# Performance work log

Measured on AMD Instinct MI355X. Metric: run time of the kernel, lower is better.

The kernel has to match this reference:

```python
import jax, jax.numpy as jnp
import numpy as np

B, L, D = 2048, 100, 128          # batch, early_cycle_threshold, d_model
F = L * D                          # flattened curve features = 12800
DLLM, DFF, E, K = 768, 256, 8, 2   # d_llm, d_ff, num_experts, top_k
EPS = 1e-9


def setup_inputs() -> dict:
    key = jax.random.key(0)
    ks = jax.random.split(key, 12)
    gin = DLLM + 1 + F  # gate input dim: concat(DKP, cycle_number, flat curve)
    return {
        "cycle_curve_data": jax.random.normal(ks[0], (B, L, D), jnp.float32),
        "cycle_numbers": jax.random.uniform(ks[1], (B, 1), jnp.float32) * 100.0,
        "DKP_embeddings": jax.random.normal(ks[2], (B, DLLM), jnp.float32),
        # gate MLP (PatternRouter_three): concat -> d_ff -> gelu -> num_experts
        "Wg1": jax.random.normal(ks[3], (gin, DFF), jnp.float32) / np.sqrt(gin),
        "bg1": jnp.zeros((DFF,), jnp.float32),
        "Wg2": jax.random.normal(ks[4], (DFF, E), jnp.float32) / np.sqrt(DFF),
        "bg2": jnp.zeros((E,), jnp.float32),
        # per-expert Linear(F, d_model)
        "We": jax.random.normal(ks[5], (E, F, D), jnp.float32) / np.sqrt(F),
        "be": jnp.zeros((E, D), jnp.float32),
        # general expert Linear(F, d_model)
        "Wgen": jax.random.normal(ks[6], (F, D), jnp.float32) / np.sqrt(F),
        "bgen": jnp.zeros((D,), jnp.float32),
    }


def reference(cycle_curve_data, cycle_numbers, DKP_embeddings,
              Wg1, bg1, Wg2, bg2, We, be, Wgen, bgen):
    b = cycle_curve_data.shape[0]
    xf = cycle_curve_data.reshape(b, -1)  # [B, F]

    # gate logits: MLP on concat(DKP, cycle_numbers, flattened curve)
    gin = jnp.concatenate([DKP_embeddings, cycle_numbers, xf], axis=-1)
    h = jax.nn.gelu(gin @ Wg1 + bg1)
    logits = h @ Wg2 + bg2                # [B, E]

    # top-k mask, softmax over ALL experts, then mask + renormalize
    _, idx = jax.lax.top_k(logits, K)     # [B, K]
    mask = jnp.sum(jax.nn.one_hot(idx, E, dtype=logits.dtype), axis=1)  # [B, E]
    probs = jax.nn.softmax(logits, axis=-1)
    masked = probs * mask
    gates = masked / (jnp.sum(masked, axis=-1, keepdims=True) + EPS)  # [B, E]

    # experts: dense compute, zero gates nullify unselected experts (same math
    # as gather-compute-scatter dispatch/combine)
    expert_outs = jnp.einsum('bf,efd->bed', xf, We) + be   # [B, E, D]
    combined = jnp.einsum('be,bed->bd', gates, expert_outs)
    combined = combined.astype(jnp.bfloat16)               # torch .to(bfloat16)

    general = xf @ Wgen + bgen                              # [B, D] f32
    final_out = general + combined.astype(general.dtype)    # bf16+f32 -> f32
    return final_out
```

## Files before the change

kernel.cpp:

```cpp
#include <hip/hip_runtime.h>
#include <hip/hip_bf16.h>
#include <stdint.h>

#define B_    2048
#define F_    12800
#define DLLM_ 768
#define E_    8
#define G1Z   32
#define MKSPLIT 8
#define MKPER (F_ / MKSPLIT)
#define BK    64

typedef __bf16 bf16x8 __attribute__((ext_vector_type(8)));
typedef float  f32x4  __attribute__((ext_vector_type(4)));

__device__ __forceinline__ unsigned short f2bf(float f) {
    unsigned int u = __float_as_uint(f);
    u += 0x7fffu + ((u >> 16) & 1u);
    return (unsigned short)(u >> 16);
}

__global__ __launch_bounds__(256) void k_convert(const float* __restrict__ src,
                                                 unsigned short* __restrict__ dst, int n4) {
    int i = blockIdx.x * 256 + threadIdx.x;
    if (i >= n4) return;
    float4 v = ((const float4*)src)[i];
    ushort4 o;
    o.x = f2bf(v.x); o.y = f2bf(v.y); o.z = f2bf(v.z); o.w = f2bf(v.w);
    ((ushort4*)dst)[i] = o;
}

__global__ __launch_bounds__(256) void k_transpose_bf16(const float* __restrict__ We,
                                                        const float* __restrict__ Wgen,
                                                        unsigned short* __restrict__ WeT,
                                                        unsigned short* __restrict__ WgenT) {
    __shared__ float t[32][33];
    int z = blockIdx.z;
    const float* src = (z < 8) ? (We + (size_t)z * F_ * 128) : Wgen;
    unsigned short* dst = (z < 8) ? (WeT + (size_t)z * 128 * F_) : WgenT;
    int k0 = blockIdx.x * 32, n0 = blockIdx.y * 32;
    int tx = threadIdx.x, ty = threadIdx.y;
#pragma unroll
    for (int i = 0; i < 4; i++) {
        int k = k0 + ty + i * 8;
        t[ty + i * 8][tx] = src[(size_t)k * 128 + n0 + tx];
    }
    __syncthreads();
#pragma unroll
    for (int i = 0; i < 4; i++) {
        int n = n0 + ty + i * 8;
        dst[(size_t)n * F_ + k0 + tx] = f2bf(t[tx][ty + i * 8]);
    }
}

__global__ __launch_bounds__(256, 2) void k_gate1(const float* __restrict__ dkp,
                                                  const float* __restrict__ xf,
                                                  const float* __restrict__ Wg1,
                                                  float* __restrict__ h_part,
                                                  int nparts) {
    __shared__ float As[16][132];
    __shared__ float Bs[16][260];
    int m0 = blockIdx.x * 128;
    int s = blockIdx.y;
    int it0 = s * 26 + (s < 16 ? s : 16);
    int nit = 26 + (s < 16 ? 1 : 0);
    int t = threadIdx.x;
    int tm = t >> 5;
    int tn = t & 31;

    float acc[16][8];
#pragma unroll
    for (int i = 0; i < 16; i++)
#pragma unroll
        for (int j = 0; j < 8; j++) acc[i][j] = 0.f;

    int arow = t >> 2, akq = (t & 3) * 4;
    int bkr = t >> 6, bcol = (t & 63) * 4;

    float4 aR[2], bR[4];
    auto preload = [&](int k) {
        const float* Ab; int astr, aoff, wr0;
        if (k < DLLM_) { Ab = dkp; astr = DLLM_; aoff = k; wr0 = k; }
        else           { Ab = xf;  astr = F_;    aoff = k - DLLM_; wr0 = k + 1; }
        aR[0] = *(const float4*)&Ab[(size_t)(m0 + arow) * astr + aoff + akq];
        aR[1] = *(const float4*)&Ab[(size_t)(m0 + arow + 64) * astr + aoff + akq];
#pragma unroll
        for (int r = 0; r < 4; r++)
            bR[r] = *(const float4*)&Wg1[(size_t)(wr0 + bkr + r * 4) * 256 + bcol];
    };
    preload(it0 * 16);
    for (int it = 0; it < nit; it++) {
        __syncthreads();
        {
            float a0[4] = {aR[0].x, aR[0].y, aR[0].z, aR[0].w};
            float a1[4] = {aR[1].x, aR[1].y, aR[1].z, aR[1].w};
#pragma unroll
            for (int j = 0; j < 4; j++) {
                As[akq + j][arow]      = a0[j];
                As[akq + j][arow + 64] = a1[j];
            }
#pragma unroll
            for (int r = 0; r < 4; r++)
                *(float4*)&Bs[bkr + r * 4][bcol] = bR[r];
        }
        __syncthreads();
        if (it + 1 < nit) preload((it0 + it + 1) * 16);
#pragma unroll 4
        for (int kk = 0; kk < 16; kk++) {
            float4 a0 = *(const float4*)&As[kk][tm * 16];
            float4 a1 = *(const float4*)&As[kk][tm * 16 + 4];
            float4 a2 = *(const float4*)&As[kk][tm * 16 + 8];
            float4 a3 = *(const float4*)&As[kk][tm * 16 + 12];
            float4 b0 = *(const float4*)&Bs[kk][tn * 8];
            float4 b1 = *(const float4*)&Bs[kk][tn * 8 + 4];
            float av[16] = {a0.x, a0.y, a0.z, a0.w, a1.x, a1.y, a1.z, a1.w,
                            a2.x, a2.y, a2.z, a2.w, a3.x, a3.y, a3.z, a3.w};
            float bv[8]  = {b0.x, b0.y, b0.z, b0.w, b1.x, b1.y, b1.z, b1.w};
#pragma unroll
            for (int i = 0; i < 16; i++)
#pragma unroll
                for (int j = 0; j < 8; j++) acc[i][j] = fmaf(av[i], bv[j], acc[i][j]);
        }
    }
    if (nparts > 1) {
        float* dst = h_part + (size_t)s * B_ * 256;
#pragma unroll
        for (int i = 0; i < 16; i++) {
            size_t base = (size_t)(m0 + tm * 16 + i) * 256 + tn * 8;
            *(float4*)&dst[base]     = (float4){acc[i][0], acc[i][1], acc[i][2], acc[i][3]};
            *(float4*)&dst[base + 4] = (float4){acc[i][4], acc[i][5], acc[i][6], acc[i][7]};
        }
    } else {
#pragma unroll
        for (int i = 0; i < 16; i++) {
            size_t base = (size_t)(m0 + tm * 16 + i) * 256 + tn * 8;
#pragma unroll
            for (int j = 0; j < 8; j++) atomicAdd(&h_part[base + j], acc[i][j]);
        }
    }
}

__global__ __launch_bounds__(256) void k_gate2(const float* __restrict__ h_part,
                                               const float* __restrict__ cyc,
                                               const float* __restrict__ Wg1,
                                               const float* __restrict__ bg1,
                                               const float* __restrict__ Wg2,
                                               const float* __restrict__ bg2,
                                               float* __restrict__ gates,
                                               unsigned int* __restrict__ cnt,
                                               unsigned int* __restrict__ rows,
                                               int nparts) {
    __shared__ float hs[8 * 257];
    __shared__ float w2s[256 * 8];
    __shared__ float ls[8][9];
    int r0 = blockIdx.x * 8;
    int t = threadIdx.x;
    const float* w768 = Wg1 + (size_t)DLLM_ * 256;
    float wc = w768[t], b1c = bg1[t];
#pragma unroll
    for (int i = 0; i < 8; i++) {
        size_t idx = (size_t)(r0 + i) * 256 + t;
        float x = 0.f;
        for (int p = 0; p < nparts; p++) x += h_part[(size_t)p * B_ * 256 + idx];
        x += cyc[r0 + i] * wc + b1c;
        float x3 = x * x * x;
        float g = 0.5f * x * (1.f + tanhf(0.7978845608028654f * (x + 0.044715f * x3)));
        hs[i * 257 + t] = g;
    }
#pragma unroll
    for (int i = 0; i < 8; i++) w2s[i * 256 + t] = Wg2[i * 256 + t];
    __syncthreads();
    if (t < 64) {
        int r = t >> 3, e = t & 7;
        float s = bg2[e];
        for (int k2 = 0; k2 < 256; k2++) s = fmaf(hs[r * 257 + k2], w2s[k2 * 8 + e], s);
        ls[r][e] = s;
    }
    __syncthreads();
    if (t < 8) {
        float l[8];
#pragma unroll
        for (int e = 0; e < 8; e++) l[e] = ls[t][e];
        int i1 = 0; float v1 = l[0];
#pragma unroll
        for (int e = 1; e < 8; e++) if (l[e] > v1) { v1 = l[e]; i1 = e; }
        int i2 = -1; float v2 = -3.0e38f;
#pragma unroll
        for (int e = 0; e < 8; e++) if (e != i1 && l[e] > v2) { v2 = l[e]; i2 = e; }
        float p[8], ps = 0.f;
#pragma unroll
        for (int e = 0; e < 8; e++) { p[e] = expf(l[e] - v1); ps += p[e]; }
        float msum = (p[i1] + p[i2]) / ps;
        float gi = 1.f / (msum + 1e-9f);
        int row = r0 + t;
#pragma unroll
        for (int e = 0; e < 8; e++) {
            float ge = (e == i1 || e == i2) ? (p[e] / ps) * gi : 0.f;
            gates[row * 8 + e] = ge;
        }
        unsigned int s1 = atomicAdd(&cnt[i1], 1u); rows[i1 * 2048 + s1] = (unsigned int)row;
        unsigned int s2 = atomicAdd(&cnt[i2], 1u); rows[i2 * 2048 + s2] = (unsigned int)row;
    }
}

__global__ __launch_bounds__(256) void k_moe(const unsigned short* __restrict__ xfb,
                                             const unsigned short* __restrict__ WeT,
                                             const unsigned short* __restrict__ WgenT,
                                             const float* __restrict__ be,
                                             const float* __restrict__ gates,
                                             const unsigned int* __restrict__ cnt,
                                             const unsigned int* __restrict__ rows,
                                             float* __restrict__ comb,
                                             float* __restrict__ gen) {
    __shared__ unsigned short As[64 * 72];
    __shared__ unsigned short Bs[128 * 72];
    __shared__ unsigned int rowid_s[64];
    int e = blockIdx.y, tile = blockIdx.x, split = blockIdx.z;
    int n_rows = (e < 8) ? (int)cnt[e] : 2048;
    if (tile * 64 >= n_rows) return;
    int t = threadIdx.x;
    if (t < 64) {
        int m = tile * 64 + t;
        unsigned int row = (e < 8) ? ((m < n_rows) ? rows[e * 2048 + m] : rows[e * 2048])
                                   : (unsigned int)m;
        rowid_s[t] = row;
    }
    __syncthreads();
    const unsigned short* WT = (e < 8) ? (WeT + (size_t)e * 128 * F_) : WgenT;
    int k0 = split * MKPER;

    int arow = t >> 2, akq = t & 3;
    const unsigned short* aptr = xfb + (size_t)rowid_s[arow] * F_ + k0 + akq * 8;
    unsigned short* asd0 = &As[arow * 72 + akq * 8];
    unsigned short* asd1 = &As[arow * 72 + (akq + 4) * 8];
    int bcol = t >> 1, bh = t & 1;
    const unsigned short* bptr = WT + (size_t)bcol * F_ + k0 + bh * 32;
    unsigned short* bsd = &Bs[bcol * 72 + bh * 32];

    int lane = t & 63;
    int lm = lane & 15, lg = lane >> 4;
    int wave = t >> 6, wr = wave >> 1, wc2 = wave & 1;

    f32x4 acc[2][4];
#pragma unroll
    for (int i = 0; i < 2; i++)
#pragma unroll
        for (int j = 0; j < 4; j++) acc[i][j] = (f32x4){0.f, 0.f, 0.f, 0.f};

    uint4 ra0 = *(const uint4*)aptr;
    uint4 ra1 = *(const uint4*)(aptr + 32);
    uint4 rb0 = *(const uint4*)(bptr);
    uint4 rb1 = *(const uint4*)(bptr + 8);
    uint4 rb2 = *(const uint4*)(bptr + 16);
    uint4 rb3 = *(const uint4*)(bptr + 24);
    for (int kk = 0; kk < MKPER; kk += BK) {
        __syncthreads();
        *(uint4*)asd0 = ra0;
        *(uint4*)asd1 = ra1;
        *(uint4*)(bsd)      = rb0;
        *(uint4*)(bsd + 8)  = rb1;
        *(uint4*)(bsd + 16) = rb2;
        *(uint4*)(bsd + 24) = rb3;
        __syncthreads();
        if (kk + BK < MKPER) {
            aptr += BK; bptr += BK;
            ra0 = *(const uint4*)aptr;
            ra1 = *(const uint4*)(aptr + 32);
            rb0 = *(const uint4*)(bptr);
            rb1 = *(const uint4*)(bptr + 8);
            rb2 = *(const uint4*)(bptr + 16);
            rb3 = *(const uint4*)(bptr + 24);
        }
#pragma unroll
        for (int kb = 0; kb < 2; kb++) {
            bf16x8 af[2], bfr[4];
#pragma unroll
            for (int mt = 0; mt < 2; mt++)
                af[mt] = *(const bf16x8*)&As[(wr * 32 + mt * 16 + lm) * 72 + (kb * 4 + lg) * 8];
#pragma unroll
            for (int nt = 0; nt < 4; nt++)
                bfr[nt] = *(const bf16x8*)&Bs[(wc2 * 64 + nt * 16 + lm) * 72 + (kb * 4 + lg) * 8];
#pragma unroll
            for (int mt = 0; mt < 2; mt++)
#pragma unroll
                for (int nt = 0; nt < 4; nt++)
                    acc[mt][nt] = __builtin_amdgcn_mfma_f32_16x16x32_bf16(af[mt], bfr[nt], acc[mt][nt], 0, 0, 0);
        }
    }
#pragma unroll
    for (int mt = 0; mt < 2; mt++) {
        int rl0 = wr * 32 + mt * 16 + lg * 4;
#pragma unroll
        for (int nt = 0; nt < 4; nt++) {
            int col = wc2 * 64 + nt * 16 + lm;
#pragma unroll
            for (int r = 0; r < 4; r++) {
                int rloc = rl0 + r;
                float v = acc[mt][nt][r];
                if (e < 8) {
                    if (tile * 64 + rloc < n_rows) {
                        unsigned int grow = rowid_s[rloc];
                        float g = gates[grow * 8 + e];
                        float bias = (split == 0) ? be[e * 128 + col] : 0.f;
                        atomicAdd(&comb[(size_t)grow * 128 + col], g * (v + bias));
                    }
                } else {
                    atomicAdd(&gen[(size_t)(tile * 64 + rloc) * 128 + col], v);
                }
            }
        }
    }
}

__global__ __launch_bounds__(256) void k_final(const float* __restrict__ gen,
                                               const float* __restrict__ comb,
                                               const float* __restrict__ bgen,
                                               float* __restrict__ out) {
    int i = blockIdx.x * 256 + threadIdx.x;
    float g = gen[i] + bgen[i & 127];
    unsigned short cb = f2bf(comb[i]);
    float c = __uint_as_float(((unsigned int)cb) << 16);
    out[i] = g + c;
}

extern "C" void kernel_launch(void* const* d_in, const int* in_sizes, int n_in,
                              void* d_out, int out_size, void* d_ws, size_t ws_size,
                              hipStream_t stream) {
    (void)in_sizes; (void)n_in; (void)out_size;
    const float* ccd  = (const float*)d_in[0];
    const float* cyc  = (const float*)d_in[1];
    const float* dkp  = (const float*)d_in[2];
    const float* Wg1  = (const float*)d_in[3];
    const float* bg1  = (const float*)d_in[4];
    const float* Wg2  = (const float*)d_in[5];
    const float* bg2  = (const float*)d_in[6];
    const float* We   = (const float*)d_in[7];
    const float* be   = (const float*)d_in[8];
    const float* Wgen = (const float*)d_in[9];
    const float* bgen = (const float*)d_in[10];
    float* out = (float*)d_out;

    char* ws = (char*)d_ws;
    size_t o = 0;
    unsigned short* xfb   = (unsigned short*)(ws + o); o += (size_t)B_ * F_ * 2;
    unsigned short* WeT   = (unsigned short*)(ws + o); o += (size_t)E_ * 128 * F_ * 2;
    unsigned short* WgenT = (unsigned short*)(ws + o); o += (size_t)128 * F_ * 2;
    float* gates = (float*)(ws + o); o += (size_t)B_ * 8 * 4;
    unsigned int* cnt = (unsigned int*)(ws + o); o += 256;
    unsigned int* rows = (unsigned int*)(ws + o); o += (size_t)8 * 2048 * 4;
    float* comb = (float*)(ws + o); o += (size_t)B_ * 128 * 4;
    float* gen  = (float*)(ws + o); o += (size_t)B_ * 128 * 4;
    float* h_part = (float*)(ws + o);
    size_t need_full = o + (size_t)G1Z * B_ * 256 * 4;
    int nparts = (ws_size >= need_full) ? G1Z : 1;

    if (nparts == 1)
        hipMemsetAsync(h_part, 0, (size_t)B_ * 256 * 4, stream);
    hipMemsetAsync(comb, 0, (size_t)B_ * 128 * 4, stream);
    hipMemsetAsync(gen,  0, (size_t)B_ * 128 * 4, stream);
    hipMemsetAsync(cnt,  0, 32, stream);

    k_convert<<<(B_ * F_ / 4) / 256, 256, 0, stream>>>(ccd, xfb, B_ * F_ / 4);
    k_transpose_bf16<<<dim3(F_ / 32, 4, 9), dim3(32, 8, 1), 0, stream>>>(We, Wgen, WeT, WgenT);
    k_gate1<<<dim3(16, G1Z), 256, 0, stream>>>(dkp, ccd, Wg1, h_part, nparts);
    k_gate2<<<B_ / 8, 256, 0, stream>>>(h_part, cyc, Wg1, bg1, Wg2, bg2, gates, cnt, rows, nparts);
    k_moe<<<dim3(32, 9, MKSPLIT), 256, 0, stream>>>(xfb, WeT, WgenT, be, gates, cnt, rows, comb, gen);
    k_final<<<(B_ * 128) / 256, 256, 0, stream>>>(gen, comb, bgen, out);
}
```

Measured before the change: 652.1 us.

## Replace MoE atomics with per-split partial buffers and remap gate1 B-tile columns

The MoE kernel now writes split-K and top-k-slot partial results into separate buffers, reusing the gate partial region, instead of doing atomicAdd into comb/gen. The final kernel sums 16 comb partials and 8 gen partials. The row index is tagged with a slot bit so each row's two expert contributions land in distinct buffers. Gate1's per-thread B columns change from 8 contiguous to two groups of 4, which avoids LDS bank conflicts and gives coalesced stores. This removes atomic contention and the memsets, at the cost of extra partial-buffer traffic in the final kernel.

```diff
diff --git a/kernel.cpp b/kernel.cpp
--- a/kernel.cpp
+++ b/kernel.cpp
@@ -111,8 +111,8 @@
             float4 a1 = *(const float4*)&As[kk][tm * 16 + 4];
             float4 a2 = *(const float4*)&As[kk][tm * 16 + 8];
             float4 a3 = *(const float4*)&As[kk][tm * 16 + 12];
-            float4 b0 = *(const float4*)&Bs[kk][tn * 8];
-            float4 b1 = *(const float4*)&Bs[kk][tn * 8 + 4];
+            float4 b0 = *(const float4*)&Bs[kk][tn * 4];
+            float4 b1 = *(const float4*)&Bs[kk][128 + tn * 4];
             float av[16] = {a0.x, a0.y, a0.z, a0.w, a1.x, a1.y, a1.z, a1.w,
                             a2.x, a2.y, a2.z, a2.w, a3.x, a3.y, a3.z, a3.w};
             float bv[8]  = {b0.x, b0.y, b0.z, b0.w, b1.x, b1.y, b1.z, b1.w};
@@ -126,16 +126,18 @@
         float* dst = h_part + (size_t)s * B_ * 256;
 #pragma unroll
         for (int i = 0; i < 16; i++) {
-            size_t base = (size_t)(m0 + tm * 16 + i) * 256 + tn * 8;
-            *(float4*)&dst[base]     = (float4){acc[i][0], acc[i][1], acc[i][2], acc[i][3]};
-            *(float4*)&dst[base + 4] = (float4){acc[i][4], acc[i][5], acc[i][6], acc[i][7]};
+            size_t base = (size_t)(m0 + tm * 16 + i) * 256;
+            *(float4*)&dst[base + tn * 4]       = (float4){acc[i][0], acc[i][1], acc[i][2], acc[i][3]};
+            *(float4*)&dst[base + 128 + tn * 4] = (float4){acc[i][4], acc[i][5], acc[i][6], acc[i][7]};
         }
     } else {
 #pragma unroll
         for (int i = 0; i < 16; i++) {
-            size_t base = (size_t)(m0 + tm * 16 + i) * 256 + tn * 8;
-#pragma unroll
-            for (int j = 0; j < 8; j++) atomicAdd(&h_part[base + j], acc[i][j]);
+            size_t base = (size_t)(m0 + tm * 16 + i) * 256;
+#pragma unroll
+            for (int j = 0; j < 4; j++) atomicAdd(&h_part[base + tn * 4 + j], acc[i][j]);
+#pragma unroll
+            for (int j = 4; j < 8; j++) atomicAdd(&h_part[base + 128 + tn * 4 + j - 4], acc[i][j]);
         }
     }
 }
@@ -199,7 +201,7 @@
             gates[row * 8 + e] = ge;
         }
         unsigned int s1 = atomicAdd(&cnt[i1], 1u); rows[i1 * 2048 + s1] = (unsigned int)row;
-        unsigned int s2 = atomicAdd(&cnt[i2], 1u); rows[i2 * 2048 + s2] = (unsigned int)row;
+        unsigned int s2 = atomicAdd(&cnt[i2], 1u); rows[i2 * 2048 + s2] = (unsigned int)row | 0x10000u;
     }
 }
 
@@ -210,8 +212,9 @@
                                              const float* __restrict__ gates,
                                              const unsigned int* __restrict__ cnt,
                                              const unsigned int* __restrict__ rows,
-                                             float* __restrict__ comb,
-                                             float* __restrict__ gen) {
+                                             float* __restrict__ comb_part,
+                                             float* __restrict__ gen_part,
+                                             int pflag) {
     __shared__ unsigned short As[64 * 72];
     __shared__ unsigned short Bs[128 * 72];
     __shared__ unsigned int rowid_s[64];
@@ -221,16 +224,16 @@
     int t = threadIdx.x;
     if (t < 64) {
         int m = tile * 64 + t;
-        unsigned int row = (e < 8) ? ((m < n_rows) ? rows[e * 2048 + m] : rows[e * 2048])
-                                   : (unsigned int)m;
-        rowid_s[t] = row;
+        unsigned int entry = (e < 8) ? ((m < n_rows) ? rows[e * 2048 + m] : rows[e * 2048])
+                                     : (unsigned int)m;
+        rowid_s[t] = entry;
     }
     __syncthreads();
     const unsigned short* WT = (e < 8) ? (WeT + (size_t)e * 128 * F_) : WgenT;
     int k0 = split * MKPER;
 
     int arow = t >> 2, akq = t & 3;
-    const unsigned short* aptr = xfb + (size_t)rowid_s[arow] * F_ + k0 + akq * 8;
+    const unsigned short* aptr = xfb + (size_t)(rowid_s[arow] & 0xFFFFu) * F_ + k0 + akq * 8;
     unsigned short* asd0 = &As[arow * 72 + akq * 8];
     unsigned short* asd1 = &As[arow * 72 + (akq + 4) * 8];
     int bcol = t >> 1, bh = t & 1;
@@ -299,28 +302,47 @@
                 float v = acc[mt][nt][r];
                 if (e < 8) {
                     if (tile * 64 + rloc < n_rows) {
-                        unsigned int grow = rowid_s[rloc];
+                        unsigned int entry = rowid_s[rloc];
+                        unsigned int grow = entry & 0xFFFFu;
+                        unsigned int slot = entry >> 16;
                         float g = gates[grow * 8 + e];
                         float bias = (split == 0) ? be[e * 128 + col] : 0.f;
-                        atomicAdd(&comb[(size_t)grow * 128 + col], g * (v + bias));
+                        float val = g * (v + bias);
+                        if (pflag)
+                            comb_part[((size_t)(split * 2 + slot) * B_ + grow) * 128 + col] = val;
+                        else
+                            atomicAdd(&comb_part[(size_t)grow * 128 + col], val);
                     }
                 } else {
-                    atomicAdd(&gen[(size_t)(tile * 64 + rloc) * 128 + col], v);
+                    int row = tile * 64 + rloc;
+                    if (pflag)
+                        gen_part[((size_t)split * B_ + row) * 128 + col] = v;
+                    else
+                        atomicAdd(&gen_part[(size_t)row * 128 + col], v);
                 }
             }
         }
     }
 }
 
-__global__ __launch_bounds__(256) void k_final(const float* __restrict__ gen,
-                                               const float* __restrict__ comb,
+__global__ __launch_bounds__(256) void k_final(const float* __restrict__ gen_part,
+                                               const float* __restrict__ comb_part,
                                                const float* __restrict__ bgen,
-                                               float* __restrict__ out) {
+                                               float* __restrict__ out, int pflag) {
     int i = blockIdx.x * 256 + threadIdx.x;
-    float g = gen[i] + bgen[i & 127];
-    unsigned short cb = f2bf(comb[i]);
-    float c = __uint_as_float(((unsigned int)cb) << 16);
-    out[i] = g + c;
+    float c = 0.f, g = 0.f;
+    if (pflag) {
+#pragma unroll
+        for (int p = 0; p < 16; p++) c += comb_part[(size_t)p * B_ * 128 + i];
+#pragma unroll
+        for (int p = 0; p < 8; p++) g += gen_part[(size_t)p * B_ * 128 + i];
+    } else {
+        c = comb_part[i];
+        g = gen_part[i];
+    }
+    unsigned short cb = f2bf(c);
+    float cf = __uint_as_float(((unsigned int)cb) << 16);
+    out[i] = g + bgen[i & 127] + cf;
 }
 
 extern "C" void kernel_launch(void* const* d_in, const int* in_sizes, int n_in,
@@ -348,22 +370,28 @@
     float* gates = (float*)(ws + o); o += (size_t)B_ * 8 * 4;
     unsigned int* cnt = (unsigned int*)(ws + o); o += 256;
     unsigned int* rows = (unsigned int*)(ws + o); o += (size_t)8 * 2048 * 4;
-    float* comb = (float*)(ws + o); o += (size_t)B_ * 128 * 4;
-    float* gen  = (float*)(ws + o); o += (size_t)B_ * 128 * 4;
-    float* h_part = (float*)(ws + o);
-    size_t need_full = o + (size_t)G1Z * B_ * 256 * 4;
-    int nparts = (ws_size >= need_full) ? G1Z : 1;
+    char* R = ws + o;
+    float* h_part    = (float*)R;
+    float* comb_part = (float*)R;
+    float* gen_part  = (float*)(R + (size_t)16 * B_ * 128 * 4);
+    size_t need_gate  = o + (size_t)G1Z * B_ * 256 * 4;
+    size_t need_moe   = o + (size_t)24 * B_ * 128 * 4;
+    int nparts = (ws_size >= need_gate) ? G1Z : 1;
+    int pflag  = (ws_size >= need_moe) ? 1 : 0;
 
     if (nparts == 1)
         hipMemsetAsync(h_part, 0, (size_t)B_ * 256 * 4, stream);
-    hipMemsetAsync(comb, 0, (size_t)B_ * 128 * 4, stream);
-    hipMemsetAsync(gen,  0, (size_t)B_ * 128 * 4, stream);
-    hipMemsetAsync(cnt,  0, 32, stream);
+    hipMemsetAsync(cnt, 0, 32, stream);
 
     k_convert<<<(B_ * F_ / 4) / 256, 256, 0, stream>>>(ccd, xfb, B_ * F_ / 4);
     k_transpose_bf16<<<dim3(F_ / 32, 4, 9), dim3(32, 8, 1), 0, stream>>>(We, Wgen, WeT, WgenT);
     k_gate1<<<dim3(16, G1Z), 256, 0, stream>>>(dkp, ccd, Wg1, h_part, nparts);
     k_gate2<<<B_ / 8, 256, 0, stream>>>(h_part, cyc, Wg1, bg1, Wg2, bg2, gates, cnt, rows, nparts);
-    k_moe<<<dim3(32, 9, MKSPLIT), 256, 0, stream>>>(xfb, WeT, WgenT, be, gates, cnt, rows, comb, gen);
-    k_final<<<(B_ * 128) / 256, 256, 0, stream>>>(gen, comb, bgen, out);
-}
+    if (!pflag) {
+        hipMemsetAsync(comb_part, 0, (size_t)B_ * 128 * 4, stream);
+        hipMemsetAsync(gen_part,  0, (size_t)B_ * 128 * 4, stream);
+    }
+    k_moe<<<dim3(32, 9, MKSPLIT), 256, 0, stream>>>(xfb, WeT, WgenT, be, gates, cnt, rows,
+                                                    comb_part, gen_part, pflag);
+    k_final<<<(B_ * 128) / 256, 256, 0, stream>>>(gen_part, comb_part, bgen, out, pflag);
+}
```

After: 637.1 us. 1.02x faster.
